# Performance work log

Hardware: AMD Instinct MI355X
Metric: run time of the kernel (lower is better)

## Reference

```python
import jax, jax.numpy as jnp
import numpy as np

B, T, D, H, LORA = 4, 1024, 1024, 16, 64
HD = D // H
BLOCK_ID, N_BLOCKS = 6, 12


def _ln(x, w, b, eps=1e-5):
    m = x.mean(-1, keepdims=True)
    v = ((x - m) ** 2).mean(-1, keepdims=True)
    return (x - m) * jax.lax.rsqrt(v + eps) * w + b


def _lora(z, a, b, l):
    return l + jnp.tanh(z @ a.T) @ b.T


def setup_inputs() -> dict:
    key = jax.random.key(0)
    ks = iter(jax.random.split(key, 64))
    rn = lambda shape, s: jax.random.normal(next(ks), shape, jnp.float32) * s
    inp = {}
    inp['x'] = rn((B, T, D), 1.0)
    r1 = 1.0 - BLOCK_ID / N_BLOCKS
    i = np.arange(D)
    inp['xw'] = jnp.asarray(1.0 - (i / D) ** r1, jnp.float32)
    for nm in ('rW', 'kW', 'vW', 'gW'):
        inp[nm] = rn((D, D), 0.02)
    for p in ('r', 'k', 'v', 'g', 'd'):
        inp[p + '_la'] = rn((LORA, D), 0.001)
        inp[p + '_lb'] = rn((D, LORA), 0.001)
        inp[p + '_ll'] = rn((D,), 1.0)
    inp['ln_w'] = jnp.full((HD,), ((1 + BLOCK_ID) / N_BLOCKS) ** 0.7, jnp.float32)
    inp['ln_b'] = jnp.zeros((HD,), jnp.float32)
    inp['oW'] = rn((D, D), 0.02)
    inp['init_state'] = rn((H, HD, HD), 1.0)
    r0 = BLOCK_ID / (N_BLOCKS - 1)
    ih = i % HD
    inp['u'] = jnp.asarray(r0 * (1 - ih / (D - 1)) + np.remainder(0.1 * (ih + 1), 3.0), jnp.float32)
    return inp


def reference(x, xw, rW, kW, vW, gW, r_la, r_lb, r_ll, k_la, k_lb, k_ll,
              v_la, v_lb, v_ll, g_la, g_lb, g_ll, d_la, d_lb, d_ll,
              ln_w, ln_b, oW, init_state, u):
    b, t, d = x.shape
    h = init_state.shape[0]
    hd = d // h
    # token shift: xx[t] = x[t-1], xx[0] = 0
    xx = jnp.concatenate([jnp.zeros_like(x[:, :1]), x[:, :-1]], axis=1)
    dx = xx - x
    lerpx = x + dx * xw
    r = (x + dx * _lora(lerpx, r_la, r_lb, r_ll)) @ rW.T
    k = (x + dx * _lora(lerpx, k_la, k_lb, k_ll)) @ kW.T
    v = (x + dx * _lora(lerpx, v_la, v_lb, v_ll)) @ vW.T
    g = (x + dx * _lora(lerpx, g_la, g_lb, g_ll)) @ gW.T
    w = jnp.exp(-jnp.exp(_lora(x + dx * _lora(lerpx, d_la, d_lb, d_ll), d_la, d_lb, d_ll)))
    # [B,T,D] -> [T,B,H,hd] for the time scan
    split = lambda z: z.reshape(b, t, h, hd).transpose(1, 0, 2, 3)
    rs, ws, ks, vs = split(r), split(w), split(k), split(v)
    uh = u.reshape(h, hd)
    st0 = jnp.broadcast_to(init_state, (b, h, hd, hd))

    def step(st, inp):
        rt, wt, kt, vt = inp
        kv = jnp.einsum('bhi,bhj->bhij', kt, vt)      # outer product
        y = jnp.einsum('bhi,bhij->bhj', rt, st + uh[None, :, :, None] * kv)
        return wt[..., None] * st + kv, y             # diag(w) @ S + kv

    st1, ys = jax.lax.scan(step, st0, (rs, ws, ks, vs))  # ys: [T,B,H,hd]
    o = jax.nn.silu(g.reshape(b, t, h, hd)) * _ln(ys.transpose(1, 0, 2, 3), ln_w, ln_b)
    return o.reshape(b, t, d) @ oW.T, st1
```

## Files before the change

### kernel.cpp

```cpp
#include <hip/hip_runtime.h>
#include <hip/hip_bf16.h>

typedef unsigned short u16;
typedef unsigned int u32;
typedef __attribute__((ext_vector_type(2))) float f32x2;
typedef __attribute__((ext_vector_type(4))) float f32x4;
typedef __attribute__((ext_vector_type(8))) short s16x8;

#define AS1 __attribute__((address_space(1)))
#define AS3 __attribute__((address_space(3)))

#define NB 4
#define TTOK 1024
#define DD 1024
#define NH 16
#define HD 64
#define MT 4096
#define NCH 16
#define CLEN 64

static __device__ __forceinline__ float b2f(u16 u) {
  union { unsigned int u; float f; } c; c.u = ((unsigned int)u) << 16; return c.f;
}
static __device__ __forceinline__ u16 f2b(float f) {
  union { float f; unsigned int u; } c; c.f = f;
  return (u16)((c.u + 0x7fffu + ((c.u >> 16) & 1u)) >> 16);
}
static __device__ __forceinline__ void gload16(const u16* g, u16* l) {
  __builtin_amdgcn_global_load_lds((const AS1 u32*)g, (AS3 u32*)l, 16, 0, 0);
}
static __device__ __forceinline__ int swz(int lin) {
  return lin ^ (((lin >> 9) & 3) << 5) ^ (((lin >> 7) & 1) << 4);
}

__global__ __launch_bounds__(256) void convW(const float* __restrict__ s0, const float* __restrict__ s1,
                                             const float* __restrict__ s2, const float* __restrict__ s3,
                                             const float* __restrict__ s4, u16* __restrict__ dst) {
  long f = ((long)blockIdx.x * 256 + threadIdx.x) << 2;
  int sel = (int)(f >> 20);
  const float* s = sel == 0 ? s0 : sel == 1 ? s1 : sel == 2 ? s2 : sel == 3 ? s3 : s4;
  long off = f & 1048575;
  f32x4 v = *(const f32x4*)&s[off];
  ushort4 o; o.x = f2b(v[0]); o.y = f2b(v[1]); o.z = f2b(v[2]); o.w = f2b(v[3]);
  *(ushort4*)&dst[f] = o;
}

__global__ __launch_bounds__(256) void convLora(
    const float* a0, const float* a1, const float* a2, const float* a3, const float* a4,
    const float* b0, const float* b1, const float* b2, const float* b3, const float* b4,
    const float* l0, const float* l1, const float* l2, const float* l3, const float* l4,
    u16* __restrict__ laD, u16* __restrict__ lbD, float* __restrict__ llD) {
  long f = ((long)blockIdx.x * 256 + threadIdx.x) << 2;
  if (f < 327680) {
    int sel = (int)(f >> 16); long off = f & 65535;
    const float* s = sel == 0 ? a0 : sel == 1 ? a1 : sel == 2 ? a2 : sel == 3 ? a3 : a4;
    f32x4 v = *(const f32x4*)&s[off];
    ushort4 o; o.x = f2b(v[0]); o.y = f2b(v[1]); o.z = f2b(v[2]); o.w = f2b(v[3]);
    *(ushort4*)&laD[f] = o;
  } else if (f < 655360) {
    long g = f - 327680;
    int sel = (int)(g >> 16); long off = g & 65535;
    const float* s = sel == 0 ? b0 : sel == 1 ? b1 : sel == 2 ? b2 : sel == 3 ? b3 : b4;
    f32x4 v = *(const f32x4*)&s[off];
    ushort4 o; o.x = f2b(v[0]); o.y = f2b(v[1]); o.z = f2b(v[2]); o.w = f2b(v[3]);
    *(ushort4*)&lbD[g] = o;
  } else if (f < 660480) {
    long g = f - 655360;
    int sel = (int)(g >> 10); long off = g & 1023;
    const float* s = sel == 0 ? l0 : sel == 1 ? l1 : sel == 2 ? l2 : sel == 3 ? l3 : l4;
    *(f32x4*)&llD[g] = *(const f32x4*)&s[off];
  }
}

__global__ __launch_bounds__(256) void prep(const float* __restrict__ x, const float* __restrict__ xw,
                                            u16* __restrict__ lerpx, u16* __restrict__ xB,
                                            u16* __restrict__ dxB) {
  long f = ((long)blockIdx.x * 256 + threadIdx.x) << 2;
  int d = (int)(f & (DD - 1));
  int m = (int)(f >> 10);
  int t = m & (TTOK - 1);
  f32x4 xv = *(const f32x4*)&x[f];
  f32x4 xm = {};
  if (t > 0) xm = *(const f32x4*)&x[f - DD];
  f32x4 xwv = *(const f32x4*)&xw[d];
  f32x4 dx = xm - xv;
  f32x4 lp = xv + dx * xwv;
  ushort4 o; o.x = f2b(lp[0]); o.y = f2b(lp[1]); o.z = f2b(lp[2]); o.w = f2b(lp[3]);
  *(ushort4*)&lerpx[f] = o;
  ushort4 ox; ox.x = f2b(xv[0]); ox.y = f2b(xv[1]); ox.z = f2b(xv[2]); ox.w = f2b(xv[3]);
  *(ushort4*)&xB[f] = ox;
  ushort4 od; od.x = f2b(dx[0]); od.y = f2b(dx[1]); od.z = f2b(dx[2]); od.w = f2b(dx[3]);
  *(ushort4*)&dxB[f] = od;
}

template<int BM, int BN, int EPI>
__launch_bounds__(256)
__global__ void gemm2(const u16* __restrict__ Ab, long sAz,
                      const u16* __restrict__ Bb, long sBz,
                      void* __restrict__ Ob, long sOz,
                      const float* __restrict__ llb,
                      const u16* __restrict__ xB,
                      const u16* __restrict__ dxB,
                      int M, int N, int K) {
  __shared__ __align__(16) u16 As[BM * 64];
  __shared__ __align__(16) u16 Bs[BN * 64];
  const int z = blockIdx.z;
  const u16* A = Ab + (long)z * sAz;
  const u16* Bw = Bb + (long)z * sBz;
  const int m0 = blockIdx.x * BM;
  const int n0 = blockIdx.y * BN;
  const int tid = threadIdx.x;
  const int l = tid & 63;
  const int wv = tid >> 6;
  constexpr int WM = BM / 2, WN = BN / 2;
  constexpr int FM = WM / 16, FN = WN / 16;
  const int wm0 = (wv >> 1) * WM, wn0 = (wv & 1) * WN;
  const int lrow = l & 15, lk = (l >> 4) * 8;
  constexpr int GA = BM / 32, GB = BN / 32;
  int gA[GA], gB[GB];
#pragma unroll
  for (int q = 0; q < GA; ++q) {
    int d = (q * 256 + tid) * 16;
    int bb = swz(d);
    gA[q] = (m0 + (bb >> 7)) * K + ((bb & 127) >> 1);
  }
#pragma unroll
  for (int q = 0; q < GB; ++q) {
    int d = (q * 256 + tid) * 16;
    int bb = swz(d);
    gB[q] = (n0 + (bb >> 7)) * K + ((bb & 127) >> 1);
  }
  int aOff[FM][2], bOff[FN][2];
#pragma unroll
  for (int m = 0; m < FM; ++m)
#pragma unroll
    for (int kk = 0; kk < 2; ++kk)
      aOff[m][kk] = swz(((wm0 + m * 16 + lrow) << 7) + (kk << 6) + (lk << 1));
#pragma unroll
  for (int n = 0; n < FN; ++n)
#pragma unroll
    for (int kk = 0; kk < 2; ++kk)
      bOff[n][kk] = swz(((wn0 + n * 16 + lrow) << 7) + (kk << 6) + (lk << 1));
  f32x4 acc[FM][FN] = {};
  for (int k0 = 0; k0 < K; k0 += 64) {
    __syncthreads();
#pragma unroll
    for (int q = 0; q < GA; ++q)
      gload16(&A[(long)gA[q] + k0], (u16*)((char*)As + (q * 256 + tid) * 16));
#pragma unroll
    for (int q = 0; q < GB; ++q)
      gload16(&Bw[(long)gB[q] + k0], (u16*)((char*)Bs + (q * 256 + tid) * 16));
    __syncthreads();
#pragma unroll
    for (int kk = 0; kk < 2; ++kk) {
      s16x8 af[FM], bfr[FN];
#pragma unroll
      for (int m = 0; m < FM; ++m) af[m] = *(const s16x8*)((const char*)As + aOff[m][kk]);
#pragma unroll
      for (int n = 0; n < FN; ++n) bfr[n] = *(const s16x8*)((const char*)Bs + bOff[n][kk]);
#pragma unroll
      for (int m = 0; m < FM; ++m)
#pragma unroll
        for (int n = 0; n < FN; ++n)
          acc[m][n] = __builtin_amdgcn_mfma_f32_16x16x32_bf16(af[m], bfr[n], acc[m][n], 0, 0, 0);
    }
  }
#pragma unroll
  for (int m = 0; m < FM; ++m) {
#pragma unroll
    for (int n = 0; n < FN; ++n) {
      const int j = n0 + wn0 + n * 16 + lrow;
#pragma unroll
      for (int q = 0; q < 4; ++q) {
        const int i = m0 + wm0 + m * 16 + (l >> 4) * 4 + q;
        const long off = (long)i * N + j;
        float v = acc[m][n][q];
        if constexpr (EPI == 0) {
          ((float*)Ob + (long)z * sOz)[off] = v;
        } else if constexpr (EPI == 1) {
          ((u16*)Ob + (long)z * sOz)[off] = f2b(tanhf(v));
        } else if constexpr (EPI == 2) {
          float val = b2f(xB[off]) + b2f(dxB[off]) * (llb[(long)z * N + j] + v);
          ((u16*)Ob + (long)z * sOz)[off] = f2b(val);
        } else if constexpr (EPI == 3) {
          ((float*)Ob + (long)z * sOz)[off] = expf(-expf(llb[j] + v));
        } else {
          ((u16*)Ob + (long)z * sOz)[off] = f2b(v);
        }
      }
    }
  }
}

__global__ __launch_bounds__(512) void scan_local(
    const u16* __restrict__ rP, const u16* __restrict__ kP,
    const u16* __restrict__ vP, const float* __restrict__ wP,
    const float* __restrict__ uP, u16* __restrict__ ysB,
    u16* __restrict__ rtil, float* __restrict__ SL, float* __restrict__ AC) {
  __shared__ __align__(16) float Rf[64 * 64];
  __shared__ __align__(16) float Kf[64 * 64];
  __shared__ __align__(16) float Wf[64 * 64];
  __shared__ __align__(16) u16 Vs[64 * 64];
  __shared__ __align__(16) char Ubuf[16384];
  u16* Rt = (u16*)Ubuf;
  float* seg = (float*)(Ubuf + 12288);
  float* Y8 = (float*)Ubuf;
  const int bhc = blockIdx.x;
  const int c = bhc & (NCH - 1), h = (bhc >> 4) & (NH - 1), b = bhc >> 8;
  const int tid = threadIdx.x;
  const int l = tid & 63;
  const int wv = tid >> 6;
  const long base0 = ((long)(b * TTOK + c * CLEN) << 10) + h * HD;
  const int st = tid >> 3, sjo = (tid & 7) * 8;
  gload16(&vP[base0 + (long)st * DD + sjo], (u16*)Vs + tid * 8);
#pragma unroll
  for (int q = 0; q < 2; ++q) {
    int cidx = q * 512 + tid;
    int t = cidx >> 4, off = (cidx & 15) * 4;
    __builtin_amdgcn_global_load_lds((const AS1 u32*)&wP[base0 + (long)t * DD + off],
                                     (AS3 u32*)((float*)Wf + cidx * 4), 16, 0, 0);
  }
  {
    s16x8 rv = *(const s16x8*)&rP[base0 + (long)st * DD + sjo];
    s16x8 kv = *(const s16x8*)&kP[base0 + (long)st * DD + sjo];
    f32x4 r0, r1, k0, k1;
#pragma unroll
    for (int e = 0; e < 4; ++e) {
      r0[e] = b2f((u16)rv[e]); r1[e] = b2f((u16)rv[e + 4]);
      k0[e] = b2f((u16)kv[e]); k1[e] = b2f((u16)kv[e + 4]);
    }
    *(f32x4*)&Rf[st * 64 + sjo] = r0; *(f32x4*)&Rf[st * 64 + sjo + 4] = r1;
    *(f32x4*)&Kf[st * 64 + sjo] = k0; *(f32x4*)&Kf[st * 64 + sjo + 4] = k1;
  }
  __syncthreads();
  {
    float p = 1.f;
#pragma unroll
    for (int q = 0; q < 8; ++q) p *= Wf[(8 * wv + q) * 64 + l];
    seg[wv * 64 + l] = p;
  }
  __syncthreads();
  {
    float sv[8];
#pragma unroll
    for (int w2 = 0; w2 < 8; ++w2) sv[w2] = seg[w2 * 64 + l];
    float pre = 1.f;
    for (int w2 = 0; w2 < wv; ++w2) pre *= sv[w2];
    float a = pre;
#pragma unroll
    for (int q = 0; q < 8; ++q) {
      const int tt = 8 * wv + q;
      Rt[tt * 64 + l] = f2b(Rf[tt * 64 + l] * a);
      a *= Wf[tt * 64 + l];
    }
    if (wv == 0) {
      float all = sv[0];
#pragma unroll
      for (int w2 = 1; w2 < 8; ++w2) all *= sv[w2];
      AC[(long)bhc * 64 + l] = all;
    }
  }
  __syncthreads();
  *(s16x8*)&rtil[base0 + (long)st * DD + sjo] = *(const s16x8*)&Rt[st * 64 + sjo];
  __syncthreads();
  f32x2 u2[4];
#pragma unroll
  for (int e = 0; e < 4; ++e) u2[e] = *(const f32x2*)&uP[h * HD + 8 * wv + 2 * e];
  f32x2 s2[4] = {};
  for (int t0 = 0; t0 < CLEN; t0 += 8) {
    float y8[8];
#pragma unroll
    for (int q = 0; q < 8; ++q) {
      const int tt = t0 + q;
      const int ro = tt * 64 + 8 * wv;
      const f32x4 rA = *(const f32x4*)&Rf[ro];
      const f32x4 rB = *(const f32x4*)&Rf[ro + 4];
      const f32x4 kA = *(const f32x4*)&Kf[ro];
      const f32x4 kB = *(const f32x4*)&Kf[ro + 4];
      const f32x4 wA = *(const f32x4*)&Wf[ro];
      const f32x4 wB = *(const f32x4*)&Wf[ro + 4];
      const float vj = b2f(Vs[tt * 64 + l]);
      const f32x2 vj2 = {vj, vj};
      f32x2 y2 = {0.f, 0.f};
      {
        const f32x2 rp = {rA[0], rA[1]}, kp = {kA[0], kA[1]}, wp = {wA[0], wA[1]};
        const f32x2 kv = kp * vj2;
        y2 = __builtin_elementwise_fma(rp, __builtin_elementwise_fma(u2[0], kv, s2[0]), y2);
        s2[0] = __builtin_elementwise_fma(wp, s2[0], kv);
      }
      {
        const f32x2 rp = {rA[2], rA[3]}, kp = {kA[2], kA[3]}, wp = {wA[2], wA[3]};
        const f32x2 kv = kp * vj2;
        y2 = __builtin_elementwise_fma(rp, __builtin_elementwise_fma(u2[1], kv, s2[1]), y2);
        s2[1] = __builtin_elementwise_fma(wp, s2[1], kv);
      }
      {
        const f32x2 rp = {rB[0], rB[1]}, kp = {kB[0], kB[1]}, wp = {wB[0], wB[1]};
        const f32x2 kv = kp * vj2;
        y2 = __builtin_elementwise_fma(rp, __builtin_elementwise_fma(u2[2], kv, s2[2]), y2);
        s2[2] = __builtin_elementwise_fma(wp, s2[2], kv);
      }
      {
        const f32x2 rp = {rB[2], rB[3]}, kp = {kB[2], kB[3]}, wp = {wB[2], wB[3]};
        const f32x2 kv = kp * vj2;
        y2 = __builtin_elementwise_fma(rp, __builtin_elementwise_fma(u2[3], kv, s2[3]), y2);
        s2[3] = __builtin_elementwise_fma(wp, s2[3], kv);
      }
      y8[q] = y2[0] + y2[1];
    }
#pragma unroll
    for (int q = 0; q < 8; ++q) Y8[(wv * 8 + q) * 64 + l] = y8[q];
    __syncthreads();
    {
      float acc = Y8[wv * 64 + l];
#pragma unroll
      for (int w2 = 1; w2 < 8; ++w2) acc += Y8[(w2 * 8 + wv) * 64 + l];
      ysB[base0 + (long)(t0 + wv) * DD + l] = f2b(acc);
    }
    __syncthreads();
  }
#pragma unroll
  for (int e = 0; e < 4; ++e) {
    SL[((long)bhc * 64 + 8 * wv + 2 * e) * 64 + l] = s2[e][0];
    SL[((long)bhc * 64 + 8 * wv + 2 * e + 1) * 64 + l] = s2[e][1];
  }
}

__global__ __launch_bounds__(256) void scan_prop(
    float* __restrict__ SL, const float* __restrict__ AC,
    const float* __restrict__ initS, float* __restrict__ st1) {
  const int bh = blockIdx.x >> 2;
  const int jq = blockIdx.x & 3;
  const int h = bh & (NH - 1);
  const int i = threadIdx.x >> 2;
  const int jo = jq * 16 + (threadIdx.x & 3) * 4;
  f32x4 sin4 = *(const f32x4*)(initS + ((long)h * 64 + i) * 64 + jo);
  for (int cc = 0; cc < NCH; ++cc) {
    const long bhc = (long)bh * NCH + cc;
    f32x4* slp = (f32x4*)(SL + (bhc * 64 + i) * 64 + jo);
    const float Ai = AC[bhc * 64 + i];
    f32x4 sl = *slp;
    *slp = sin4;
    sin4 = Ai * sin4 + sl;
  }
  *(f32x4*)(st1 + ((long)bh * 64 + i) * 64 + jo) = sin4;
}

__global__ __launch_bounds__(256) void scan_corr(
    const float* __restrict__ SL, const u16* __restrict__ rtil, float* __restrict__ ysC) {
  __shared__ __align__(16) float S[64 * 64];
  const int bhc = blockIdx.x;
  const int c = bhc & (NCH - 1), h = (bhc >> 4) & (NH - 1), b = bhc >> 8;
  const int tid = threadIdx.x;
  const f32x4* sp = (const f32x4*)(SL + (long)bhc * 4096);
  for (int q = tid; q < 1024; q += 256) ((f32x4*)S)[q] = sp[q];
  __syncthreads();
  const int t = tid >> 2, jg = (tid & 3) * 16;
  const long base = ((long)(b * TTOK + c * CLEN + t) * DD) + h * HD;
  f32x4 yacc[4] = {};
  const u16* rp = rtil + base;
#pragma unroll 8
  for (int i = 0; i < 64; ++i) {
    const float r = b2f(rp[i]);
    const f32x4* srow = (const f32x4*)&S[i * 64 + jg];
#pragma unroll
    for (int e = 0; e < 4; ++e) yacc[e] += r * srow[e];
  }
  f32x4* yp = (f32x4*)(ysC + base + jg);
#pragma unroll
  for (int e = 0; e < 4; ++e) yp[e] = yacc[e];
}

__global__ __launch_bounds__(256) void ln_silu(
    const u16* __restrict__ ysB, const float* __restrict__ ysC,
    const u16* __restrict__ gP,
    const float* __restrict__ lnw, const float* __restrict__ lnb,
    u16* __restrict__ oB) {
  const int ridx = blockIdx.x * 4 + (threadIdx.x >> 6);
  const int lane = threadIdx.x & 63;
  const long basem = (long)ridx * 64;
  const float y = b2f(ysB[basem + lane]) + ysC[basem + lane];
  float su = y, sq = y * y;
#pragma unroll
  for (int msk = 1; msk < 64; msk <<= 1) {
    su += __shfl_xor(su, msk, 64);
    sq += __shfl_xor(sq, msk, 64);
  }
  const float mean = su * (1.f / 64.f);
  const float var = sq * (1.f / 64.f) - mean * mean;
  const float rs = rsqrtf(var + 1e-5f);
  const float g = b2f(gP[basem + lane]);
  const float silu = g / (1.f + expf(-g));
  const float val = silu * ((y - mean) * rs * lnw[lane] + lnb[lane]);
  oB[basem + lane] = f2b(val);
}

extern "C" void kernel_launch(void* const* d_in, const int* in_sizes, int n_in,
                              void* d_out, int out_size, void* d_ws, size_t ws_size,
                              hipStream_t stream) {
  const float* x   = (const float*)d_in[0];
  const float* xw  = (const float*)d_in[1];
  const float* rW  = (const float*)d_in[2];
  const float* kW  = (const float*)d_in[3];
  const float* vW  = (const float*)d_in[4];
  const float* gW  = (const float*)d_in[5];
  const float* r_la = (const float*)d_in[6],  *r_lb = (const float*)d_in[7],  *r_ll = (const float*)d_in[8];
  const float* k_la = (const float*)d_in[9],  *k_lb = (const float*)d_in[10], *k_ll = (const float*)d_in[11];
  const float* v_la = (const float*)d_in[12], *v_lb = (const float*)d_in[13], *v_ll = (const float*)d_in[14];
  const float* g_la = (const float*)d_in[15], *g_lb = (const float*)d_in[16], *g_ll = (const float*)d_in[17];
  const float* d_la = (const float*)d_in[18], *d_lb = (const float*)d_in[19], *d_ll = (const float*)d_in[20];
  const float* lnw = (const float*)d_in[21];
  const float* lnb = (const float*)d_in[22];
  const float* oW  = (const float*)d_in[23];
  const float* initS = (const float*)d_in[24];
  const float* uP  = (const float*)d_in[25];
  float* out = (float*)d_out;

  char* ws = (char*)d_ws;
  u16*   W_all  = (u16*)(ws + 0);
  u16*   la_all = (u16*)(ws + 10485760);
  u16*   lb_all = (u16*)(ws + 11141120);
  float* ll_all = (float*)(ws + 11796480);
  u16*   lerpx  = (u16*)(ws + 11816960);
  u16*   xB     = (u16*)(ws + 20205568);
  u16*   dxB    = (u16*)(ws + 28594176);
  u16*   t1_all = (u16*)(ws + 36982784);
  u16*   z_all  = (u16*)(ws + 39604224);
  u16*   rkvg   = (u16*)(ws + 81547264);
  float* wbuf   = (float*)(ws + 115101696);
  u16*   rtil   = (u16*)(ws + 131878912);
  float* SL     = (float*)(ws + 140267520);
  float* AC     = (float*)(ws + 157044736);
  u16*   ysB    = (u16*)(ws + 157306880);
  u16*   oB     = (u16*)(ws + 174084096);
  float* ysC    = (float*)(ws + 115101696);

  convW<<<5120, 256, 0, stream>>>(rW, kW, vW, gW, oW, W_all);
  convLora<<<645, 256, 0, stream>>>(r_la, k_la, v_la, g_la, d_la,
                                    r_lb, k_lb, v_lb, g_lb, d_lb,
                                    r_ll, k_ll, v_ll, g_ll, d_ll,
                                    la_all, lb_all, ll_all);
  prep<<<4096, 256, 0, stream>>>(x, xw, lerpx, xB, dxB);

  gemm2<64, 64, 1><<<dim3(64, 1, 5), 256, 0, stream>>>(
      lerpx, 0L, la_all, 65536L, (void*)t1_all, 262144L, nullptr, nullptr, nullptr, MT, 64, 1024);
  gemm2<128, 128, 2><<<dim3(32, 8, 5), 256, 0, stream>>>(
      t1_all, 262144L, lb_all, 65536L, (void*)z_all, 4194304L, ll_all, xB, dxB, MT, 1024, 64);
  gemm2<64, 64, 1><<<dim3(64, 1, 1), 256, 0, stream>>>(
      z_all + 4L * 4194304, 0L, la_all + 4L * 65536, 0L, (void*)t1_all, 0L, nullptr, nullptr, nullptr, MT, 64, 1024);
  gemm2<128, 128, 3><<<dim3(32, 8, 1), 256, 0, stream>>>(
      t1_all, 0L, lb_all + 4L * 65536, 0L, (void*)wbuf, 0L, ll_all + 4096, nullptr, nullptr, MT, 1024, 64);
  gemm2<128, 128, 4><<<dim3(32, 8, 4), 256, 0, stream>>>(
      z_all, 4194304L, W_all, 1048576L, (void*)rkvg, 4194304L, nullptr, nullptr, nullptr, MT, 1024, 1024);

  scan_local<<<1024, 512, 0, stream>>>(rkvg, rkvg + 4194304L, rkvg + 2L * 4194304, wbuf,
                                       uP, ysB, rtil, SL, AC);
  scan_prop<<<256, 256, 0, stream>>>(SL, AC, initS, out + 4194304);
  scan_corr<<<1024, 256, 0, stream>>>(SL, rtil, ysC);

  ln_silu<<<16384, 256, 0, stream>>>(ysB, ysC, rkvg + 3L * 4194304, lnw, lnb, oB);
  gemm2<128, 128, 0><<<dim3(32, 8, 1), 256, 0, stream>>>(
      oB, 0L, W_all + 4L * 1048576, 0L, (void*)out, 0L, nullptr, nullptr, nullptr, MT, 1024, 1024);
}
```

Before: 349.2 us.

## Add 256x256-tile double-buffered GEMM kernel for projection and output GEMMs

```diff
diff --git a/kernel.cpp b/kernel.cpp
--- a/kernel.cpp
+++ b/kernel.cpp
@@ -31,6 +31,9 @@
 }
 static __device__ __forceinline__ int swz(int lin) {
   return lin ^ (((lin >> 9) & 3) << 5) ^ (((lin >> 7) & 1) << 4);
+}
+static __device__ __forceinline__ int swz16x32(int b) {
+  return b ^ (((b >> 9) & 1) << 5);
 }
 
 __global__ __launch_bounds__(256) void convW(const float* __restrict__ s0, const float* __restrict__ s1,
@@ -186,6 +189,105 @@
           ((float*)Ob + (long)z * sOz)[off] = expf(-expf(llb[j] + v));
         } else {
           ((u16*)Ob + (long)z * sOz)[off] = f2b(v);
+        }
+      }
+    }
+  }
+}
+
+template<int EPI>
+__launch_bounds__(512, 1)
+__global__ void gemm256(const u16* __restrict__ Ab, long sAz,
+                        const u16* __restrict__ Bb, long sBz,
+                        void* __restrict__ Ob, long sOz,
+                        int M, int N, int K) {
+  __shared__ __align__(16) u16 LB[2][2][16384];
+  const int z = blockIdx.z;
+  const u16* A = Ab + (long)z * sAz;
+  const u16* Bw = Bb + (long)z * sBz;
+  const int m0 = blockIdx.x * 256;
+  const int n0 = blockIdx.y * 256;
+  const int tid = threadIdx.x;
+  const int l = tid & 63;
+  const int wid = tid >> 6;
+  const int wr = wid >> 2, wc = wid & 3;
+  const int lrow = l & 15, lkb = (l >> 4) * 16;
+  long gA[4], gB[4];
+#pragma unroll
+  for (int q = 0; q < 4; ++q) {
+    int d = (q * 512 + tid) * 16;
+    int s = swz16x32(d);
+    gA[q] = (long)(m0 + (s >> 7)) * K + ((s & 127) >> 1);
+    gB[q] = (long)(n0 + (s >> 7)) * K + ((s & 127) >> 1);
+  }
+  int aOff[8][2], bOff[4][2];
+#pragma unroll
+  for (int m = 0; m < 8; ++m)
+#pragma unroll
+    for (int kk = 0; kk < 2; ++kk)
+      aOff[m][kk] = swz16x32((wr * 128 + m * 16 + lrow) * 128 + kk * 64 + lkb);
+#pragma unroll
+  for (int n = 0; n < 4; ++n)
+#pragma unroll
+    for (int kk = 0; kk < 2; ++kk)
+      bOff[n][kk] = swz16x32((wc * 64 + n * 16 + lrow) * 128 + kk * 64 + lkb);
+  const int ktiles = K >> 6;
+#pragma unroll
+  for (int q = 0; q < 4; ++q) gload16(&A[gA[q]], &LB[0][0][0] + (q * 512 + tid) * 8);
+#pragma unroll
+  for (int q = 0; q < 4; ++q) gload16(&Bw[gB[q]], &LB[0][1][0] + (q * 512 + tid) * 8);
+  if (ktiles > 1) {
+#pragma unroll
+    for (int q = 0; q < 4; ++q) gload16(&A[gA[q] + 64], &LB[1][0][0] + (q * 512 + tid) * 8);
+#pragma unroll
+    for (int q = 0; q < 4; ++q) gload16(&Bw[gB[q] + 64], &LB[1][1][0] + (q * 512 + tid) * 8);
+  }
+  f32x4 acc[8][4] = {};
+  for (int kt = 0; kt < ktiles; ++kt) {
+    const int cur = kt & 1;
+    if (kt + 1 < ktiles) asm volatile("s_waitcnt vmcnt(8)" ::: "memory");
+    else                 asm volatile("s_waitcnt vmcnt(0)" ::: "memory");
+    __builtin_amdgcn_s_barrier();
+    const char* Ab2 = (const char*)&LB[cur][0][0];
+    const char* Bb2 = (const char*)&LB[cur][1][0];
+#pragma unroll
+    for (int kk = 0; kk < 2; ++kk) {
+      s16x8 af[8], bf[4];
+#pragma unroll
+      for (int m = 0; m < 8; ++m) af[m] = *(const s16x8*)(Ab2 + aOff[m][kk]);
+#pragma unroll
+      for (int n = 0; n < 4; ++n) bf[n] = *(const s16x8*)(Bb2 + bOff[n][kk]);
+      __builtin_amdgcn_s_setprio(1);
+#pragma unroll
+      for (int m = 0; m < 8; ++m)
+#pragma unroll
+        for (int n = 0; n < 4; ++n)
+          acc[m][n] = __builtin_amdgcn_mfma_f32_16x16x32_bf16(af[m], bf[n], acc[m][n], 0, 0, 0);
+      __builtin_amdgcn_s_setprio(0);
+    }
+    __builtin_amdgcn_s_barrier();
+    if (kt + 2 < ktiles) {
+      const int k0 = (kt + 2) * 64;
+#pragma unroll
+      for (int q = 0; q < 4; ++q) gload16(&A[gA[q] + k0], &LB[cur][0][0] + (q * 512 + tid) * 8);
+#pragma unroll
+      for (int q = 0; q < 4; ++q) gload16(&Bw[gB[q] + k0], &LB[cur][1][0] + (q * 512 + tid) * 8);
+    }
+  }
+  const int lq4 = (l >> 4) * 4;
+#pragma unroll
+  for (int m = 0; m < 8; ++m) {
+#pragma unroll
+    for (int n = 0; n < 4; ++n) {
+      const int j = n0 + wc * 64 + n * 16 + lrow;
+#pragma unroll
+      for (int q = 0; q < 4; ++q) {
+        const int i = m0 + wr * 128 + m * 16 + lq4 + q;
+        const long off = (long)i * N + j;
+        if constexpr (EPI == 0) {
+          ((float*)Ob + (long)z * sOz)[off] = acc[m][n][q];
+        } else {
+          ((u16*)Ob + (long)z * sOz)[off] = f2b(acc[m][n][q]);
         }
       }
     }
@@ -450,8 +552,8 @@
       z_all + 4L * 4194304, 0L, la_all + 4L * 65536, 0L, (void*)t1_all, 0L, nullptr, nullptr, nullptr, MT, 64, 1024);
   gemm2<128, 128, 3><<<dim3(32, 8, 1), 256, 0, stream>>>(
       t1_all, 0L, lb_all + 4L * 65536, 0L, (void*)wbuf, 0L, ll_all + 4096, nullptr, nullptr, MT, 1024, 64);
-  gemm2<128, 128, 4><<<dim3(32, 8, 4), 256, 0, stream>>>(
-      z_all, 4194304L, W_all, 1048576L, (void*)rkvg, 4194304L, nullptr, nullptr, nullptr, MT, 1024, 1024);
+  gemm256<4><<<dim3(16, 4, 4), 512, 0, stream>>>(
+      z_all, 4194304L, W_all, 1048576L, (void*)rkvg, 4194304L, MT, 1024, 1024);
 
   scan_local<<<1024, 512, 0, stream>>>(rkvg, rkvg + 4194304L, rkvg + 2L * 4194304, wbuf,
                                        uP, ysB, rtil, SL, AC);
@@ -459,6 +561,6 @@
   scan_corr<<<1024, 256, 0, stream>>>(SL, rtil, ysC);
 
   ln_silu<<<16384, 256, 0, stream>>>(ysB, ysC, rkvg + 3L * 4194304, lnw, lnb, oB);
-  gemm2<128, 128, 0><<<dim3(32, 8, 1), 256, 0, stream>>>(
-      oB, 0L, W_all + 4L * 1048576, 0L, (void*)out, 0L, nullptr, nullptr, nullptr, MT, 1024, 1024);
-}
+  gemm256<0><<<dim3(16, 4, 1), 512, 0, stream>>>(
+      oB, 0L, W_all + 4L * 1048576, 0L, (void*)out, 0L, MT, 1024, 1024);
+}
```

New measurement: 359.9 us. +3.1%, slower.
